# Kernel optimization log

Hardware: AMD Instinct MI355X
Metric: run time of the kernel (lower is better)

The kernel has to match this reference:

```python
import jax, jax.numpy as jnp
import numpy as np
import math

C_IN, C_OUT = 256, 256
KH, KW = 3, 3
STRIDE, PAD = 1, 1
CURV = 1.0
SQRT_C = math.sqrt(CURV)
EPS = 1e-15

def _beta(a, b):
    return math.exp(math.lgamma(a) + math.lgamma(b) - math.lgamma(a + b))

BETA_NI = _beta(C_IN / 2.0, 0.5)                 # beta(n_i/2, 1/2)
BETA_N = _beta(C_IN * KH * KW / 2.0, 0.5)        # beta(n/2, 1/2)


def logmap0(y, axis):
    n = jnp.maximum(jnp.linalg.norm(y, axis=axis, keepdims=True), EPS)
    return jnp.arctanh(jnp.minimum(SQRT_C * n, 1.0 - 1e-7)) * y / (SQRT_C * n)


def expmap0(v, axis):
    n = jnp.maximum(jnp.linalg.norm(v, axis=axis, keepdims=True), EPS)
    return jnp.tanh(SQRT_C * n) * v / (SQRT_C * n)


def unfold(x):
    # torch.nn.Unfold: x [B,C,H,W] -> [B, C*KH*KW, L], channel-major patch order
    B, C, H, W = x.shape
    Ho = (H + 2 * PAD - KH) // STRIDE + 1
    Wo = (W + 2 * PAD - KW) // STRIDE + 1
    xp = jnp.pad(x, ((0, 0), (0, 0), (PAD, PAD), (PAD, PAD)))
    cols = [xp[:, :, i:i + STRIDE * Ho:STRIDE, j:j + STRIDE * Wo:STRIDE]
            for i in range(KH) for j in range(KW)]
    patches = jnp.stack(cols, axis=2)            # [B, C, KH*KW, Ho, Wo]
    return patches.reshape(B, C * KH * KW, Ho * Wo), Ho, Wo


def poincare_fc(x, z, r):
    # x: [..., D_in] on ball, z: [D_in, D_out], r: [D_out]
    x2 = jnp.sum(x * x, axis=-1, keepdims=True)
    lam = 2.0 / (1.0 - CURV * x2)                # conformal factor lambda_x
    z_norm = jnp.maximum(jnp.linalg.norm(z, axis=0), EPS)  # [D_out]
    xz = x @ z                                   # [..., D_out]
    two_csr = 2.0 * SQRT_C * r
    inner = (SQRT_C * lam * xz / z_norm * jnp.cosh(two_csr)
             - (lam - 1.0) * jnp.sinh(two_csr))
    v = 2.0 * z_norm / SQRT_C * jnp.arcsinh(inner)   # hyperplane distances
    w = jnp.sinh(SQRT_C * v) / SQRT_C
    return w / (1.0 + jnp.sqrt(1.0 + CURV * jnp.sum(w * w, axis=-1, keepdims=True)))


def setup_inputs() -> dict:
    key = jax.random.key(0)
    k1, k2, k3 = jax.random.split(key, 3)
    # tangent vectors -> points on the Poincare ball (man_dim=1)
    v = 0.05 * jax.random.normal(k1, (16, C_IN, 64, 64), dtype=jnp.float32)
    x = expmap0(v, axis=1)
    std = (2.0 * C_IN * KH * KW * C_OUT) ** (-0.5)
    weights = std * jax.random.normal(k2, (KH * KW * C_IN, C_OUT), dtype=jnp.float32)
    bias = 0.01 * jax.random.normal(k3, (C_OUT,), dtype=jnp.float32)
    return {"x": x, "weights": weights, "bias": bias}


def reference(x, weights, bias):
    B = x.shape[0]
    v = logmap0(x, axis=1) * (BETA_N / BETA_NI)      # log map + beta scaling
    u, Ho, Wo = unfold(v)                            # [B, CK, L]
    u = jnp.swapaxes(u, 1, 2)                        # [B, L, CK]
    p = expmap0(u, axis=-1)                          # back onto the ball
    y = poincare_fc(p, weights, bias)                # [B, L, C_OUT]
    return jnp.swapaxes(y, 1, 2).reshape(B, C_OUT, Ho, Wo)
```

## Files before the change

kernel.cpp:

```cpp
#include <hip/hip_runtime.h>
#include <cmath>

typedef __bf16 bf16;
typedef __bf16 bf16x8 __attribute__((ext_vector_type(8)));
typedef float f32x4 __attribute__((ext_vector_type(4)));

#define SBAR() __builtin_amdgcn_sched_barrier(0)


__device__ inline void gload16(const void* g, void* l) {
    __builtin_amdgcn_global_load_lds(
        (const __attribute__((address_space(1))) unsigned int*)g,
        (__attribute__((address_space(3))) unsigned int*)l, 16, 0, 0);
}

__global__ void k_prep_zt(const float* __restrict__ z, bf16* __restrict__ zt5) {
    int s = blockIdx.x;
    int cc = s / 9, tap = s % 9;
    int co = threadIdx.x;
#pragma unroll
    for (int g = 0; g < 4; ++g) {
        bf16x8 pk;
#pragma unroll
        for (int e = 0; e < 8; ++e) {
            int c = cc * 32 + g * 8 + e;
            pk[e] = (bf16)z[(size_t)(c * 9 + tap) * 256 + co];
        }
        *(bf16x8*)(zt5 + ((size_t)(s * 4 + g) * 256 + co) * 8) = pk;
    }
}

__global__ void k_prep_cols(const float* __restrict__ z, const float* __restrict__ r,
                            float* __restrict__ zn, float* __restrict__ ch,
                            float* __restrict__ sh) {
    __shared__ float red[256];
    int co = blockIdx.x, t = threadIdx.x;
    float s = 0.f;
    for (int i = 0; i < 9; ++i) {
        float v = z[(size_t)(i * 256 + t) * 256 + co];
        s += v * v;
    }
    red[t] = s;
    __syncthreads();
    for (int off = 128; off >= 1; off >>= 1) {
        if (t < off) red[t] += red[t + off];
        __syncthreads();
    }
    if (t == 0) {
        zn[co] = fmaxf(sqrtf(red[0]), 1e-15f);
        float tc = 2.f * r[co];
        ch[co] = coshf(tc);
        sh[co] = sinhf(tc);
    }
}

__global__ void k_logmap(const float* __restrict__ x, unsigned int* __restrict__ vt_u,
                         float* __restrict__ sq, float Rbeta) {
    __shared__ float tile[256][33];
    __shared__ float red[8][32];
    __shared__ float afac[32];
    int tid = threadIdx.x;
    int blk = blockIdx.x;
    int b = blk >> 7;
    int pix0 = (blk & 127) << 5;

    for (int it = 0; it < 32; ++it) {
        int c = it * 8 + (tid >> 5);
        int p = tid & 31;
        tile[c][p] = x[((size_t)b * 256 + c) * 4096 + pix0 + p];
    }
    __syncthreads();

    {
        int part = tid >> 5, p = tid & 31;
        float s = 0.f;
        for (int i = 0; i < 32; ++i) {
            float v = tile[part * 32 + i][p];
            s += v * v;
        }
        red[part][p] = s;
    }
    __syncthreads();
    if (tid < 32) {
        float n2 = 0.f;
        for (int i = 0; i < 8; ++i) n2 += red[i][tid];
        float n = sqrtf(n2);
        float nc = fmaxf(n, 1e-15f);
        float a = atanhf(fminf(nc, 0.9999999f)) / nc * Rbeta;
        afac[tid] = a;
        sq[(size_t)b * 4096 + pix0 + tid] = a * a * n2;
    }
    __syncthreads();

    for (int it = 0; it < 16; ++it) {
        int idx = it * 256 + tid;
        int p = idx >> 7;
        int cp = idx & 127;
        float a = afac[p];
        float v0 = a * tile[2 * cp][p];
        float v1 = a * tile[2 * cp + 1][p];
        union { bf16 h[2]; unsigned int u; } pk;
        pk.h[0] = (bf16)v0;
        pk.h[1] = (bf16)v1;
        vt_u[((size_t)b * 4096 + pix0 + p) * 128 + cp] = pk.u;
    }
}

__global__ void k_boxsum(const float* __restrict__ sq, float* __restrict__ nusq) {
    int idx = blockIdx.x * 256 + threadIdx.x;
    int b = idx >> 12, hw = idx & 4095, h = hw >> 6, w = hw & 63;
    const float* s = sq + ((size_t)b << 12);
    float acc = 0.f;
    for (int dh = -1; dh <= 1; ++dh) {
        int hh = h + dh;
        if ((unsigned)hh >= 64u) continue;
        for (int dw = -1; dw <= 1; ++dw) {
            int ww = w + dw;
            if ((unsigned)ww >= 64u) continue;
            acc += s[hh * 64 + ww];
        }
    }
    nusq[idx] = acc;
}

__global__ void
__attribute__((amdgpu_flat_work_group_size(512, 512)))
__attribute__((amdgpu_waves_per_eu(2, 2)))
k_hconv(const bf16* __restrict__ vt, const bf16* __restrict__ zt5,
        const float* __restrict__ nusq,
        const float* __restrict__ znp, const float* __restrict__ chp,
        const float* __restrict__ shp, float* __restrict__ out) {
    __shared__ __align__(1024) char Asb[2][25344];
    __shared__ __align__(1024) char Bsb[2][16448];
    __shared__ float s_lds[256], lam_lds[256];
    __shared__ float red[256][2];

    int tid = threadIdx.x;
    int bid = blockIdx.x;
    int bh = ((bid & 7) << 5) | (bid >> 3);
    int b = bh >> 4, h0 = (bh & 15) << 2;

    if (tid < 96) {
        int buf = tid / 48, rem = tid % 48;
        int u = rem >> 1, side = rem & 1;
        *(f32x4*)(Asb[buf] + u * 1056 + side * 1040) = (f32x4){0.f, 0.f, 0.f, 0.f};
    }

    if (tid >= 256) {
        int t = tid - 256;
        int h = h0 + (t >> 6), w = t & 63;
        float q = nusq[((size_t)b << 12) + h * 64 + w];
        float ncl = fmaxf(sqrtf(q), 1e-15f);
        float p = __expf(2.f * ncl);
        float tt = (p - 1.f) / (p + 1.f);
        s_lds[t] = tt / ncl;
        lam_lds[t] = 2.f / (1.f - tt * tt);
    }

    int wave = tid >> 6, lane = tid & 63;
    int wn = wave & 1, wm = wave >> 1;
    int lrow = lane & 15, lk = lane >> 4;

    f32x4 acc[4][8];
#pragma unroll
    for (int m = 0; m < 4; ++m)
#pragma unroll
        for (int n = 0; n < 8; ++n) acc[m][n] = (f32x4){0.f, 0.f, 0.f, 0.f};

    const bf16* vb = vt + (((size_t)b) << 12) * 256;

    auto stageA = [&](char* dst, int ccn) {
#pragma unroll
        for (int it = 0; it < 3; ++it) {
            int u = wave * 3 + it;
            int r = u >> 2, g = u & 3;
            int hr = h0 - 1 + r;
            hr = hr < 0 ? 0 : (hr > 63 ? 63 : hr);
            const bf16* gp = vb + ((size_t)(hr * 64 + lane)) * 256 + ccn * 32 + g * 8;
            gload16(gp, dst + u * 1056 + 16);
        }
    };
    auto stageB = [&](char* dst, int snext) {
        const char* src = (const char*)zt5 + (size_t)snext * 16384;
#pragma unroll
        for (int it = 0; it < 2; ++it) {
            int u = wave * 2 + it;
            gload16(src + u * 1024 + lane * 16,
                    dst + (u >> 2) * 4112 + (u & 3) * 1024);
        }
    };

    stageB((char*)Bsb[0], 0);
    stageA((char*)Asb[0], 0);
    __syncthreads();
    SBAR();

    const int aBase = lk * 1056 + lrow * 16;
    const int bBase = lk * 4112 + (wn * 128 + lrow) * 16;

#pragma unroll 1
    for (int cc = 0; cc < 8; ++cc) {
        const int par = cc & 1;
        const char* ApW = Asb[par] + aBase + wm * 4224;
        const char* BrE = Bsb[par] + bBase;
        const char* BrO = Bsb[par ^ 1] + bBase;
        char* BwE = (char*)Bsb[par ^ 1];
        char* BwO = (char*)Bsb[par];
        char* Anx = (char*)Asb[par ^ 1];
        const int sbase = cc * 9;
        const bool notlast = (cc < 7);

#pragma unroll
        for (int tap = 0; tap < 9; ++tap) {
            if (tap < 8 || notlast) stageB((tap & 1) ? BwO : BwE, sbase + tap + 1);
            if (tap == 0 && notlast) stageA(Anx, cc + 1);
            SBAR();
            if (tap < 2) {
                if (notlast) { asm volatile("s_waitcnt vmcnt(5)" ::: "memory"); }
                else         { asm volatile("s_waitcnt vmcnt(2)" ::: "memory"); }
            } else if (tap == 8) {
                if (notlast) { asm volatile("s_waitcnt vmcnt(2)" ::: "memory"); }
                else         { asm volatile("s_waitcnt vmcnt(0)" ::: "memory"); }
            } else {
                asm volatile("s_waitcnt vmcnt(2)" ::: "memory");
            }
            SBAR();
            asm volatile("s_barrier" ::: "memory");
            SBAR();

            const int dh = tap / 3 - 1, dw = tap % 3 - 1;
            int hh = h0 + wm + dh;
            if ((unsigned)hh < 64u) {
                const char* Ap = ApW;
                const char* Bp = (tap & 1) ? BrO : BrE;
                const int ao = (dh + 1) * 4224 + (dw + 1) * 16;
                bf16x8 a0 = *(const bf16x8*)(Ap + (ao));
                bf16x8 a1 = *(const bf16x8*)(Ap + (ao + 256));
                bf16x8 a2 = *(const bf16x8*)(Ap + (ao + 512));
                bf16x8 a3 = *(const bf16x8*)(Ap + (ao + 768));
#pragma unroll
                for (int nh = 0; nh < 2; ++nh) {
                    bf16x8 b0 = *(const bf16x8*)(Bp + (nh * 1024));
                    bf16x8 b1 = *(const bf16x8*)(Bp + (nh * 1024 + 256));
                    bf16x8 b2 = *(const bf16x8*)(Bp + (nh * 1024 + 512));
                    bf16x8 b3 = *(const bf16x8*)(Bp + (nh * 1024 + 768));
                    __builtin_amdgcn_s_setprio(1);
                    acc[0][nh*4+0] = __builtin_amdgcn_mfma_f32_16x16x32_bf16(a0, b0, acc[0][nh*4+0], 0, 0, 0);
                    acc[1][nh*4+0] = __builtin_amdgcn_mfma_f32_16x16x32_bf16(a1, b0, acc[1][nh*4+0], 0, 0, 0);
                    acc[2][nh*4+0] = __builtin_amdgcn_mfma_f32_16x16x32_bf16(a2, b0, acc[2][nh*4+0], 0, 0, 0);
                    acc[3][nh*4+0] = __builtin_amdgcn_mfma_f32_16x16x32_bf16(a3, b0, acc[3][nh*4+0], 0, 0, 0);
                    acc[0][nh*4+1] = __builtin_amdgcn_mfma_f32_16x16x32_bf16(a0, b1, acc[0][nh*4+1], 0, 0, 0);
                    acc[1][nh*4+1] = __builtin_amdgcn_mfma_f32_16x16x32_bf16(a1, b1, acc[1][nh*4+1], 0, 0, 0);
                    acc[2][nh*4+1] = __builtin_amdgcn_mfma_f32_16x16x32_bf16(a2, b1, acc[2][nh*4+1], 0, 0, 0);
                    acc[3][nh*4+1] = __builtin_amdgcn_mfma_f32_16x16x32_bf16(a3, b1, acc[3][nh*4+1], 0, 0, 0);
                    acc[0][nh*4+2] = __builtin_amdgcn_mfma_f32_16x16x32_bf16(a0, b2, acc[0][nh*4+2], 0, 0, 0);
                    acc[1][nh*4+2] = __builtin_amdgcn_mfma_f32_16x16x32_bf16(a1, b2, acc[1][nh*4+2], 0, 0, 0);
                    acc[2][nh*4+2] = __builtin_amdgcn_mfma_f32_16x16x32_bf16(a2, b2, acc[2][nh*4+2], 0, 0, 0);
                    acc[3][nh*4+2] = __builtin_amdgcn_mfma_f32_16x16x32_bf16(a3, b2, acc[3][nh*4+2], 0, 0, 0);
                    acc[0][nh*4+3] = __builtin_amdgcn_mfma_f32_16x16x32_bf16(a0, b3, acc[0][nh*4+3], 0, 0, 0);
                    acc[1][nh*4+3] = __builtin_amdgcn_mfma_f32_16x16x32_bf16(a1, b3, acc[1][nh*4+3], 0, 0, 0);
                    acc[2][nh*4+3] = __builtin_amdgcn_mfma_f32_16x16x32_bf16(a2, b3, acc[2][nh*4+3], 0, 0, 0);
                    acc[3][nh*4+3] = __builtin_amdgcn_mfma_f32_16x16x32_bf16(a3, b3, acc[3][nh*4+3], 0, 0, 0);
                    __builtin_amdgcn_s_setprio(0);
                }
            }
            SBAR();
            asm volatile("s_barrier" ::: "memory");
            SBAR();
        }
    }

    float cz[8], sh8[8], tz[8];
#pragma unroll
    for (int n = 0; n < 8; ++n) {
        int co = wn * 128 + n * 16 + lrow;
        float zn = znp[co];
        cz[n] = chp[co] / zn;
        sh8[n] = shp[co];
        tz[n] = 2.f * zn;
    }

#pragma unroll
    for (int m = 0; m < 4; ++m) {
#pragma unroll
        for (int r = 0; r < 4; ++r) {
            int wp = wm * 64 + m * 16 + 4 * lk + r;
            float s = s_lds[wp], lam = lam_lds[wp];
            float lm1 = lam - 1.f;
            float psum = 0.f;
#pragma unroll
            for (int n = 0; n < 8; ++n) {
                float xz = s * acc[m][n][r];
                float inner = lam * xz * cz[n] - lm1 * sh8[n];
                float as = __logf(inner + sqrtf(inner * inner + 1.f));
                float p = __expf(tz[n] * as);
                float w = 0.5f * (p - __builtin_amdgcn_rcpf(p));
                acc[m][n][r] = w;
                psum += w * w;
            }
            psum += __shfl_xor(psum, 1);
            psum += __shfl_xor(psum, 2);
            psum += __shfl_xor(psum, 4);
            psum += __shfl_xor(psum, 8);
            if (lrow == 0) red[wp][wn] = psum;
        }
    }
    __syncthreads();

    float dinv[4][4];
#pragma unroll
    for (int m = 0; m < 4; ++m)
#pragma unroll
        for (int r = 0; r < 4; ++r) {
            int wp = wm * 64 + m * 16 + 4 * lk + r;
            float tot = red[wp][0] + red[wp][1];
            dinv[m][r] = __builtin_amdgcn_rcpf(1.f + sqrtf(1.f + tot));
        }

    float* ob = out + (size_t)b * 256 * 4096 + (h0 + wm) * 64;
#pragma unroll
    for (int m = 0; m < 4; ++m) {
#pragma unroll
        for (int n = 0; n < 8; ++n) {
            int co = wn * 128 + n * 16 + lrow;
            f32x4 o;
#pragma unroll
            for (int r = 0; r < 4; ++r) o[r] = acc[m][n][r] * dinv[m][r];
            *(f32x4*)(ob + (size_t)co * 4096 + m * 16 + 4 * lk) = o;
        }
    }
}

extern "C" void kernel_launch(void* const* d_in, const int* in_sizes, int n_in,
                              void* d_out, int out_size, void* d_ws, size_t ws_size,
                              hipStream_t stream) {
    const float* x = (const float*)d_in[0];
    const float* z = (const float*)d_in[1];
    const float* r = (const float*)d_in[2];
    float* out = (float*)d_out;

    char* ws = (char*)d_ws;
    bf16* vt = (bf16*)ws;
    float* sq = (float*)(ws + 33554432);
    float* nusq = (float*)(ws + 33816576);
    bf16* zt5 = (bf16*)(ws + 34078720);
    float* zn = (float*)(ws + 35258368);
    float* ch = (float*)(ws + 35259392);
    float* sh = (float*)(ws + 35260416);
    if (ws_size < 35261440) return;

    double bni = lgamma(128.0) + lgamma(0.5) - lgamma(128.5);
    double bn = lgamma(1152.0) + lgamma(0.5) - lgamma(1152.5);
    float Rbeta = (float)exp(bn - bni);

    k_prep_zt<<<72, 256, 0, stream>>>(z, zt5);
    k_prep_cols<<<256, 256, 0, stream>>>(z, r, zn, ch, sh);
    k_logmap<<<2048, 256, 0, stream>>>(x, (unsigned int*)vt, sq, Rbeta);
    k_boxsum<<<256, 256, 0, stream>>>(sq, nusq);
    k_hconv<<<256, 512, 0, stream>>>(vt, zt5, nusq, zn, ch, sh, out);
}
```

Baseline: 144.5 us.

## Halve conv tile to two rows, triple-buffer weights, single-buffer input for occupancy

The fused hyperbolic conv kernel now processes 2 output rows per block instead of 4, so it launches 512 blocks. Eight waves split the 256 output channels four ways, which halves the accumulator registers and allows 4 waves per EU. Weight tiles rotate through three LDS buffers with one barrier per tap. The input tile is single-buffered and reloaded only after a barrier at the end of each channel chunk. The aim is higher occupancy and more blocks per CU to hide latency, at the cost of twice the weight traffic per output row and an exposed input-load stall at each chunk boundary.

```diff
diff --git a/kernel.cpp b/kernel.cpp
--- a/kernel.cpp
+++ b/kernel.cpp
@@ -125,29 +125,28 @@
 
 __global__ void
 __attribute__((amdgpu_flat_work_group_size(512, 512)))
-__attribute__((amdgpu_waves_per_eu(2, 2)))
+__attribute__((amdgpu_waves_per_eu(4, 4)))
 k_hconv(const bf16* __restrict__ vt, const bf16* __restrict__ zt5,
         const float* __restrict__ nusq,
         const float* __restrict__ znp, const float* __restrict__ chp,
         const float* __restrict__ shp, float* __restrict__ out) {
-    __shared__ __align__(1024) char Asb[2][25344];
-    __shared__ __align__(1024) char Bsb[2][16448];
-    __shared__ float s_lds[256], lam_lds[256];
-    __shared__ float red[256][2];
+    __shared__ __align__(1024) char Asb[16896];
+    __shared__ __align__(1024) char Bsb[3][16448];
+    __shared__ float s_lds[128], lam_lds[128];
+    __shared__ float red[128][4];
 
     int tid = threadIdx.x;
     int bid = blockIdx.x;
-    int bh = ((bid & 7) << 5) | (bid >> 3);
-    int b = bh >> 4, h0 = (bh & 15) << 2;
-
-    if (tid < 96) {
-        int buf = tid / 48, rem = tid % 48;
-        int u = rem >> 1, side = rem & 1;
-        *(f32x4*)(Asb[buf] + u * 1056 + side * 1040) = (f32x4){0.f, 0.f, 0.f, 0.f};
-    }
-
-    if (tid >= 256) {
-        int t = tid - 256;
+    int bh = ((bid & 7) << 6) | (bid >> 3);
+    int b = bh >> 5, h0 = (bh & 31) << 1;
+
+    if (tid < 32) {
+        int u = tid >> 1, side = tid & 1;
+        *(f32x4*)(Asb + u * 1056 + side * 1040) = (f32x4){0.f, 0.f, 0.f, 0.f};
+    }
+
+    if (tid >= 128 && tid < 256) {
+        int t = tid - 128;
         int h = h0 + (t >> 6), w = t & 63;
         float q = nusq[((size_t)b << 12) + h * 64 + w];
         float ncl = fmaxf(sqrtf(q), 1e-15f);
@@ -158,26 +157,26 @@
     }
 
     int wave = tid >> 6, lane = tid & 63;
-    int wn = wave & 1, wm = wave >> 1;
+    int wn = wave & 3, wm = wave >> 2;
     int lrow = lane & 15, lk = lane >> 4;
 
-    f32x4 acc[4][8];
+    f32x4 acc[4][4];
 #pragma unroll
     for (int m = 0; m < 4; ++m)
 #pragma unroll
-        for (int n = 0; n < 8; ++n) acc[m][n] = (f32x4){0.f, 0.f, 0.f, 0.f};
+        for (int n = 0; n < 4; ++n) acc[m][n] = (f32x4){0.f, 0.f, 0.f, 0.f};
 
     const bf16* vb = vt + (((size_t)b) << 12) * 256;
 
-    auto stageA = [&](char* dst, int ccn) {
-#pragma unroll
-        for (int it = 0; it < 3; ++it) {
-            int u = wave * 3 + it;
+    auto stageA = [&](int ccn) {
+#pragma unroll
+        for (int it = 0; it < 2; ++it) {
+            int u = wave * 2 + it;
             int r = u >> 2, g = u & 3;
             int hr = h0 - 1 + r;
             hr = hr < 0 ? 0 : (hr > 63 ? 63 : hr);
             const bf16* gp = vb + ((size_t)(hr * 64 + lane)) * 256 + ccn * 32 + g * 8;
-            gload16(gp, dst + u * 1056 + 16);
+            gload16(gp, Asb + u * 1056 + 16);
         }
     };
     auto stageB = [&](char* dst, int snext) {
@@ -191,39 +190,25 @@
     };
 
     stageB((char*)Bsb[0], 0);
-    stageA((char*)Asb[0], 0);
+    stageA(0);
     __syncthreads();
     SBAR();
 
-    const int aBase = lk * 1056 + lrow * 16;
-    const int bBase = lk * 4112 + (wn * 128 + lrow) * 16;
+    const char* ApB = Asb + lk * 1056 + lrow * 16;
+    const int bOff = lk * 4112 + wn * 1024 + lrow * 16;
 
 #pragma unroll 1
     for (int cc = 0; cc < 8; ++cc) {
-        const int par = cc & 1;
-        const char* ApW = Asb[par] + aBase + wm * 4224;
-        const char* BrE = Bsb[par] + bBase;
-        const char* BrO = Bsb[par ^ 1] + bBase;
-        char* BwE = (char*)Bsb[par ^ 1];
-        char* BwO = (char*)Bsb[par];
-        char* Anx = (char*)Asb[par ^ 1];
         const int sbase = cc * 9;
         const bool notlast = (cc < 7);
 
 #pragma unroll
         for (int tap = 0; tap < 9; ++tap) {
-            if (tap < 8 || notlast) stageB((tap & 1) ? BwO : BwE, sbase + tap + 1);
-            if (tap == 0 && notlast) stageA(Anx, cc + 1);
+            const int s = sbase + tap;
+            if (s < 71) stageB((char*)Bsb[(tap + 1) % 3], s + 1);
             SBAR();
-            if (tap < 2) {
-                if (notlast) { asm volatile("s_waitcnt vmcnt(5)" ::: "memory"); }
-                else         { asm volatile("s_waitcnt vmcnt(2)" ::: "memory"); }
-            } else if (tap == 8) {
-                if (notlast) { asm volatile("s_waitcnt vmcnt(2)" ::: "memory"); }
-                else         { asm volatile("s_waitcnt vmcnt(0)" ::: "memory"); }
-            } else {
-                asm volatile("s_waitcnt vmcnt(2)" ::: "memory");
-            }
+            if (s < 71) { asm volatile("s_waitcnt vmcnt(2)" ::: "memory"); }
+            else        { asm volatile("s_waitcnt vmcnt(0)" ::: "memory"); }
             SBAR();
             asm volatile("s_barrier" ::: "memory");
             SBAR();
@@ -231,52 +216,52 @@
             const int dh = tap / 3 - 1, dw = tap % 3 - 1;
             int hh = h0 + wm + dh;
             if ((unsigned)hh < 64u) {
-                const char* Ap = ApW;
-                const char* Bp = (tap & 1) ? BrO : BrE;
-                const int ao = (dh + 1) * 4224 + (dw + 1) * 16;
-                bf16x8 a0 = *(const bf16x8*)(Ap + (ao));
-                bf16x8 a1 = *(const bf16x8*)(Ap + (ao + 256));
-                bf16x8 a2 = *(const bf16x8*)(Ap + (ao + 512));
-                bf16x8 a3 = *(const bf16x8*)(Ap + (ao + 768));
-#pragma unroll
-                for (int nh = 0; nh < 2; ++nh) {
-                    bf16x8 b0 = *(const bf16x8*)(Bp + (nh * 1024));
-                    bf16x8 b1 = *(const bf16x8*)(Bp + (nh * 1024 + 256));
-                    bf16x8 b2 = *(const bf16x8*)(Bp + (nh * 1024 + 512));
-                    bf16x8 b3 = *(const bf16x8*)(Bp + (nh * 1024 + 768));
-                    __builtin_amdgcn_s_setprio(1);
-                    acc[0][nh*4+0] = __builtin_amdgcn_mfma_f32_16x16x32_bf16(a0, b0, acc[0][nh*4+0], 0, 0, 0);
-                    acc[1][nh*4+0] = __builtin_amdgcn_mfma_f32_16x16x32_bf16(a1, b0, acc[1][nh*4+0], 0, 0, 0);
-                    acc[2][nh*4+0] = __builtin_amdgcn_mfma_f32_16x16x32_bf16(a2, b0, acc[2][nh*4+0], 0, 0, 0);
-                    acc[3][nh*4+0] = __builtin_amdgcn_mfma_f32_16x16x32_bf16(a3, b0, acc[3][nh*4+0], 0, 0, 0);
-                    acc[0][nh*4+1] = __builtin_amdgcn_mfma_f32_16x16x32_bf16(a0, b1, acc[0][nh*4+1], 0, 0, 0);
-                    acc[1][nh*4+1] = __builtin_amdgcn_mfma_f32_16x16x32_bf16(a1, b1, acc[1][nh*4+1], 0, 0, 0);
-                    acc[2][nh*4+1] = __builtin_amdgcn_mfma_f32_16x16x32_bf16(a2, b1, acc[2][nh*4+1], 0, 0, 0);
-                    acc[3][nh*4+1] = __builtin_amdgcn_mfma_f32_16x16x32_bf16(a3, b1, acc[3][nh*4+1], 0, 0, 0);
-                    acc[0][nh*4+2] = __builtin_amdgcn_mfma_f32_16x16x32_bf16(a0, b2, acc[0][nh*4+2], 0, 0, 0);
-                    acc[1][nh*4+2] = __builtin_amdgcn_mfma_f32_16x16x32_bf16(a1, b2, acc[1][nh*4+2], 0, 0, 0);
-                    acc[2][nh*4+2] = __builtin_amdgcn_mfma_f32_16x16x32_bf16(a2, b2, acc[2][nh*4+2], 0, 0, 0);
-                    acc[3][nh*4+2] = __builtin_amdgcn_mfma_f32_16x16x32_bf16(a3, b2, acc[3][nh*4+2], 0, 0, 0);
-                    acc[0][nh*4+3] = __builtin_amdgcn_mfma_f32_16x16x32_bf16(a0, b3, acc[0][nh*4+3], 0, 0, 0);
-                    acc[1][nh*4+3] = __builtin_amdgcn_mfma_f32_16x16x32_bf16(a1, b3, acc[1][nh*4+3], 0, 0, 0);
-                    acc[2][nh*4+3] = __builtin_amdgcn_mfma_f32_16x16x32_bf16(a2, b3, acc[2][nh*4+3], 0, 0, 0);
-                    acc[3][nh*4+3] = __builtin_amdgcn_mfma_f32_16x16x32_bf16(a3, b3, acc[3][nh*4+3], 0, 0, 0);
-                    __builtin_amdgcn_s_setprio(0);
-                }
+                const char* Ap = ApB + (wm + dh + 1) * 4224 + (dw + 1) * 16;
+                const char* Bp = (const char*)Bsb[tap % 3] + bOff;
+                bf16x8 a0 = *(const bf16x8*)(Ap);
+                bf16x8 a1 = *(const bf16x8*)(Ap + 256);
+                bf16x8 a2 = *(const bf16x8*)(Ap + 512);
+                bf16x8 a3 = *(const bf16x8*)(Ap + 768);
+                bf16x8 b0 = *(const bf16x8*)(Bp);
+                bf16x8 b1 = *(const bf16x8*)(Bp + 256);
+                bf16x8 b2 = *(const bf16x8*)(Bp + 512);
+                bf16x8 b3 = *(const bf16x8*)(Bp + 768);
+                __builtin_amdgcn_s_setprio(1);
+                acc[0][0] = __builtin_amdgcn_mfma_f32_16x16x32_bf16(a0, b0, acc[0][0], 0, 0, 0);
+                acc[1][0] = __builtin_amdgcn_mfma_f32_16x16x32_bf16(a1, b0, acc[1][0], 0, 0, 0);
+                acc[2][0] = __builtin_amdgcn_mfma_f32_16x16x32_bf16(a2, b0, acc[2][0], 0, 0, 0);
+                acc[3][0] = __builtin_amdgcn_mfma_f32_16x16x32_bf16(a3, b0, acc[3][0], 0, 0, 0);
+                acc[0][1] = __builtin_amdgcn_mfma_f32_16x16x32_bf16(a0, b1, acc[0][1], 0, 0, 0);
+                acc[1][1] = __builtin_amdgcn_mfma_f32_16x16x32_bf16(a1, b1, acc[1][1], 0, 0, 0);
+                acc[2][1] = __builtin_amdgcn_mfma_f32_16x16x32_bf16(a2, b1, acc[2][1], 0, 0, 0);
+                acc[3][1] = __builtin_amdgcn_mfma_f32_16x16x32_bf16(a3, b1, acc[3][1], 0, 0, 0);
+                acc[0][2] = __builtin_amdgcn_mfma_f32_16x16x32_bf16(a0, b2, acc[0][2], 0, 0, 0);
+                acc[1][2] = __builtin_amdgcn_mfma_f32_16x16x32_bf16(a1, b2, acc[1][2], 0, 0, 0);
+                acc[2][2] = __builtin_amdgcn_mfma_f32_16x16x32_bf16(a2, b2, acc[2][2], 0, 0, 0);
+                acc[3][2] = __builtin_amdgcn_mfma_f32_16x16x32_bf16(a3, b2, acc[3][2], 0, 0, 0);
+                acc[0][3] = __builtin_amdgcn_mfma_f32_16x16x32_bf16(a0, b3, acc[0][3], 0, 0, 0);
+                acc[1][3] = __builtin_amdgcn_mfma_f32_16x16x32_bf16(a1, b3, acc[1][3], 0, 0, 0);
+                acc[2][3] = __builtin_amdgcn_mfma_f32_16x16x32_bf16(a2, b3, acc[2][3], 0, 0, 0);
+                acc[3][3] = __builtin_amdgcn_mfma_f32_16x16x32_bf16(a3, b3, acc[3][3], 0, 0, 0);
+                __builtin_amdgcn_s_setprio(0);
             }
             SBAR();
-            asm volatile("s_barrier" ::: "memory");
-            SBAR();
-        }
-    }
-
-    float cz[8], sh8[8], tz[8];
-#pragma unroll
-    for (int n = 0; n < 8; ++n) {
-        int co = wn * 128 + n * 16 + lrow;
+            if (tap == 8) {
+                asm volatile("s_barrier" ::: "memory");
+                SBAR();
+                if (notlast) stageA(cc + 1);
+                SBAR();
+            }
+        }
+    }
+
+    float cz[4], sh4[4], tz[4];
+#pragma unroll
+    for (int n = 0; n < 4; ++n) {
+        int co = wn * 64 + n * 16 + lrow;
         float zn = znp[co];
         cz[n] = chp[co] / zn;
-        sh8[n] = shp[co];
+        sh4[n] = shp[co];
         tz[n] = 2.f * zn;
     }
 
@@ -289,9 +274,9 @@
             float lm1 = lam - 1.f;
             float psum = 0.f;
 #pragma unroll
-            for (int n = 0; n < 8; ++n) {
+            for (int n = 0; n < 4; ++n) {
                 float xz = s * acc[m][n][r];
-                float inner = lam * xz * cz[n] - lm1 * sh8[n];
+                float inner = lam * xz * cz[n] - lm1 * sh4[n];
                 float as = __logf(inner + sqrtf(inner * inner + 1.f));
                 float p = __expf(tz[n] * as);
                 float w = 0.5f * (p - __builtin_amdgcn_rcpf(p));
@@ -313,7 +298,7 @@
 #pragma unroll
         for (int r = 0; r < 4; ++r) {
             int wp = wm * 64 + m * 16 + 4 * lk + r;
-            float tot = red[wp][0] + red[wp][1];
+            float tot = (red[wp][0] + red[wp][1]) + (red[wp][2] + red[wp][3]);
             dinv[m][r] = __builtin_amdgcn_rcpf(1.f + sqrtf(1.f + tot));
         }
 
@@ -321,8 +306,8 @@
 #pragma unroll
     for (int m = 0; m < 4; ++m) {
 #pragma unroll
-        for (int n = 0; n < 8; ++n) {
-            int co = wn * 128 + n * 16 + lrow;
+        for (int n = 0; n < 4; ++n) {
+            int co = wn * 64 + n * 16 + lrow;
             f32x4 o;
 #pragma unroll
             for (int r = 0; r < 4; ++r) o[r] = acc[m][n][r] * dinv[m][r];
@@ -357,5 +342,5 @@
     k_prep_cols<<<256, 256, 0, stream>>>(z, r, zn, ch, sh);
     k_logmap<<<2048, 256, 0, stream>>>(x, (unsigned int*)vt, sq, Rbeta);
     k_boxsum<<<256, 256, 0, stream>>>(sq, nusq);
-    k_hconv<<<256, 512, 0, stream>>>(vt, zt5, nusq, zn, ch, sh, out);
-}
+    k_hconv<<<512, 512, 0, stream>>>(vt, zt5, nusq, zn, ch, sh, out);
+}
```

Result: faster. 127.3 us (-12.0%).
